# Optimization experiments

Measured on AMD Instinct MI355X. Metric: run time of the kernel, lower is better.

The kernel has to match this reference:

```python
import jax, jax.numpy as jnp
import numpy as np

B, N, C = 8, 1024, 768
H = 12
D = C // H  # head_dim = 64
SCALE = D ** -0.5


def setup_inputs() -> dict:
    key = jax.random.key(0)
    k1, k2, k3 = jax.random.split(key, 3)
    x = jax.random.normal(k1, (B, N, C), dtype=jnp.float32)
    # nn.Linear(dim, 3*dim, bias=False): weight [3C, C]
    w_qkv = jax.random.normal(k2, (3 * C, C), dtype=jnp.float32) * (C ** -0.5)
    # nn.Linear(dim, dim): weight [C, C], bias [C]
    w_proj = jax.random.normal(k3, (C, C), dtype=jnp.float32) * (C ** -0.5)
    b_proj = jnp.zeros((C,), dtype=jnp.float32)
    return {"x": x, "w_qkv": w_qkv, "w_proj": w_proj, "b_proj": b_proj}


def reference(x, w_qkv, w_proj, b_proj):
    b, n, c = x.shape
    # qkv projection: [B,N,3C] -> [3,B,H,N,D]
    qkv = jnp.einsum('bnc,fc->bnf', x, w_qkv)
    qkv = qkv.reshape(b, n, 3, H, D).transpose(2, 0, 3, 1, 4)
    q, k, v = qkv[0], qkv[1], qkv[2]
    # scaled dot-product attention (q scaled as in timm: q @ k^T * scale)
    attn = jnp.einsum('bhnd,bhmd->bhnm', q, k) * SCALE
    attn = jax.nn.softmax(attn, axis=-1)
    out = jnp.einsum('bhnm,bhmd->bhnd', attn, v)  # [B,H,N,D]
    out = out.transpose(0, 2, 1, 3).reshape(b, n, c)
    # output projection
    out = jnp.einsum('bnc,oc->bno', out, w_proj) + b_proj
    return out
```

## Files before the change

### kernel.cpp

```cpp
#include <hip/hip_runtime.h>
#include <hip/hip_bf16.h>
#include <stdint.h>


typedef unsigned short u16;
typedef __attribute__((ext_vector_type(8))) short    short8;
typedef __attribute__((ext_vector_type(4))) short    short4v;
typedef __attribute__((ext_vector_type(8))) __bf16   bf16x8;
typedef __attribute__((ext_vector_type(8))) unsigned short ushort8_t;
typedef __attribute__((ext_vector_type(4))) float    f32x4;

#define QSCALE 0.18033688011112042f

__device__ __forceinline__ u16 f2bf(float f) {
  union { float f; uint32_t u; } v; v.f = f;
  uint32_t u = v.u;
  u += 0x7fffu + ((u >> 16) & 1u);
  return (u16)(u >> 16);
}

__device__ __forceinline__ uint32_t pack_bf16(float hi, float lo) {
  uint32_t a = __builtin_bit_cast(uint32_t, hi) + 0x8000u;
  uint32_t b = __builtin_bit_cast(uint32_t, lo) + 0x8000u;
  return __builtin_amdgcn_perm(a, b, 0x07060302u);
}

__device__ __forceinline__ void gl_lds16(const void* g, void* l) {
  __builtin_amdgcn_global_load_lds(
      (const __attribute__((address_space(1))) void*)g,
      (__attribute__((address_space(3))) void*)l, 16, 0, 0);
}

__device__ __forceinline__ f32x4 mfma16(short8 a, short8 b, f32x4 c) {
  return __builtin_amdgcn_mfma_f32_16x16x32_bf16(
      __builtin_bit_cast(bf16x8, a), __builtin_bit_cast(bf16x8, b), c, 0, 0, 0);
}

__device__ __forceinline__ f32x4 mfma16k16(short4v a, short4v b, f32x4 c) {
#if __has_builtin(__builtin_amdgcn_mfma_f32_16x16x16bf16_1k)
  return __builtin_amdgcn_mfma_f32_16x16x16bf16_1k(a, b, c, 0, 0, 0);
#else
  f32x4 d = c;
  asm volatile("v_mfma_f32_16x16x16_bf16 %0, %1, %2, %0"
               : "+v"(d) : "v"(a), "v"(b));
  return d;
#endif
}

__global__ void cvt3_kernel(const float* __restrict__ x, const float* __restrict__ wq,
                            const float* __restrict__ wp, u16* __restrict__ dst) {
  const int i = blockIdx.x * blockDim.x + threadIdx.x;
  constexpr int NX = 6291456 / 4, NQ = 1769472 / 4, NP = 589824 / 4;
  float4 v;
  if (i < NX)                v = ((const float4*)x)[i];
  else if (i < NX + NQ)      v = ((const float4*)wq)[i - NX];
  else if (i < NX + NQ + NP) v = ((const float4*)wp)[i - NX - NQ];
  else return;
  ushort4 o;
  o.x = f2bf(v.x); o.y = f2bf(v.y); o.z = f2bf(v.z); o.w = f2bf(v.w);
  ((ushort4*)dst)[i] = o;
}

template <int NBX, int MODE>
__global__ __launch_bounds__(256)
void gemm_bt(const u16* __restrict__ A, const u16* __restrict__ Bw,
             u16* __restrict__ Qb, u16* __restrict__ Kb, u16* __restrict__ Vtb,
             float* __restrict__ outF, const float* __restrict__ bias) {
  constexpr int K = 768;
  __shared__ union {
    struct { alignas(16) u16 A[2][128 * 32]; alignas(16) u16 B[2][128 * 32]; } st;
    alignas(16) u16 vx[4][64 * 72];
  } sm;
  const int t = threadIdx.x;
  const int lane = t & 63;
  const int w = t >> 6;
  const int col = lane & 15;
  const int quad = lane >> 4;
  const int lin = blockIdx.x;
  const int xcd = lin & 7, j = lin >> 3;
  const int mi = xcd * 8 + (j & 7);
  const int ni = j >> 3;
  const int m0 = mi * 128;
  const int n0 = ni * 128;
  const int wm = (w >> 1) * 64;
  const int wn = (w & 1) * 64;

  f32x4 acc[4][4];
#pragma unroll
  for (int i = 0; i < 4; i++)
#pragma unroll
    for (int jj = 0; jj < 4; jj++) acc[i][jj] = (f32x4){0.f, 0.f, 0.f, 0.f};

  auto stage = [&](int buf, int k0) {
#pragma unroll
    for (int i = 0; i < 2; i++) {
      const int c = t + i * 256;
      const int row = c >> 2, kc = c & 3;
      gl_lds16(A + (m0 + row) * K + k0 + kc * 8, &sm.st.A[buf][c * 8]);
      gl_lds16(Bw + (n0 + row) * K + k0 + kc * 8, &sm.st.B[buf][c * 8]);
    }
  };

  stage(0, 0);
  for (int it = 0; it < K / 32; it++) {
    const int buf = it & 1;
    __syncthreads();
    if (it < K / 32 - 1) stage(buf ^ 1, (it + 1) * 32);
    short8 af[4], bf[4];
#pragma unroll
    for (int mb = 0; mb < 4; mb++)
      af[mb] = *(const short8*)&sm.st.A[buf][(wm + mb * 16 + col) * 32 + quad * 8];
#pragma unroll
    for (int nb = 0; nb < 4; nb++)
      bf[nb] = *(const short8*)&sm.st.B[buf][(wn + nb * 16 + col) * 32 + quad * 8];
#pragma unroll
    for (int mb = 0; mb < 4; mb++)
#pragma unroll
      for (int nb = 0; nb < 4; nb++)
        acc[mb][nb] = mfma16(af[mb], bf[nb], acc[mb][nb]);
  }

  if (MODE == 0) {
    const int tsel = n0 / 768;
    if (tsel == 2) {
      __syncthreads();
      u16* vx = sm.vx[w];
      const int b = (m0 + wm) >> 10;
      const int h = (n0 + wn - 1536) >> 6;
      const int nbase = ((m0 + wm) & 1023);
#pragma unroll
      for (int mb = 0; mb < 4; mb++)
#pragma unroll
        for (int nb = 0; nb < 4; nb++) {
          const int dloc = nb * 16 + col;
          const int tok = mb * 16 + quad * 4;
          uint2 pk;
          pk.x = pack_bf16(acc[mb][nb][1], acc[mb][nb][0]);
          pk.y = pack_bf16(acc[mb][nb][3], acc[mb][nb][2]);
          *(uint2*)&vx[dloc * 72 + tok] = pk;
        }
      __builtin_amdgcn_s_waitcnt(0);
#pragma unroll
      for (int i = 0; i < 8; i++) {
        const int dloc = i * 8 + (lane >> 3);
        const int tok = (lane & 7) * 8;
        ushort8_t v = *(const ushort8_t*)&vx[dloc * 72 + tok];
        *(ushort8_t*)&Vtb[((b * 12 + h) * 64 + dloc) * 1024 + nbase + tok] = v;
      }
    } else {
      u16* dst = (tsel == 0) ? Qb : Kb;
      const float scale = (tsel == 0) ? QSCALE : 1.0f;
#pragma unroll
      for (int mb = 0; mb < 4; mb++)
#pragma unroll
        for (int nb = 0; nb < 4; nb++)
#pragma unroll
          for (int r = 0; r < 4; r++) {
            const int row = m0 + wm + mb * 16 + quad * 4 + r;
            const int cc = n0 + wn + nb * 16 + col;
            const int b = row >> 10, n = row & 1023;
            const int hd = cc - tsel * 768;
            const int h = hd >> 6, d = hd & 63;
            dst[((b * 12 + h) * 1024 + n) * 64 + d] = f2bf(acc[mb][nb][r] * scale);
          }
    }
  } else {
#pragma unroll
    for (int mb = 0; mb < 4; mb++)
#pragma unroll
      for (int nb = 0; nb < 4; nb++)
#pragma unroll
        for (int r = 0; r < 4; r++) {
          const int row = m0 + wm + mb * 16 + quad * 4 + r;
          const int cc = n0 + wn + nb * 16 + col;
          outF[(size_t)row * 768 + cc] = acc[mb][nb][r] + bias[cc];
        }
  }
}

__global__ __launch_bounds__(256, 3)
void attn_kernel(const u16* __restrict__ Qb, const u16* __restrict__ Kb,
                 const u16* __restrict__ Vtb, u16* __restrict__ attnb) {
  __shared__ alignas(16) u16 Ks[2][64 * 64];
  __shared__ alignas(16) u16 Vs[2][64 * 64];
  const int t = threadIdx.x;
  const int lane = t & 63;
  const int w = t >> 6;
  const int col = lane & 15;
  const int quad = lane >> 4;
  const int lin = blockIdx.x;
  const int xcd = lin & 7, idx = lin >> 3;
  const int bh = xcd * 12 + idx % 12;
  const int qt = idx / 12;

  const u16* Qh = Qb + bh * 65536;
  const u16* Kh = Kb + bh * 65536;
  const u16* Vh = Vtb + bh * 65536;

  const int qrow0 = qt * 128 + w * 32;
  short8 qf[2][2];
#pragma unroll
  for (int g = 0; g < 2; g++)
#pragma unroll
    for (int s = 0; s < 2; s++)
      qf[g][s] = *(const short8*)&Qh[(qrow0 + g * 16 + col) * 64 + s * 32 + quad * 8];

  f32x4 oaccT[2][4];
#pragma unroll
  for (int g = 0; g < 2; g++)
#pragma unroll
    for (int nb = 0; nb < 4; nb++) oaccT[g][nb] = (f32x4){0.f, 0.f, 0.f, 0.f};
  float lacc[2] = {0.f, 0.f};

  auto stage = [&](int buf, int kt) {
#pragma unroll
    for (int i = 0; i < 2; i++) {
      const int c = t + i * 256;
      const int row = c >> 3, jj = c & 7;
      const int js = jj ^ (row & 7);
      gl_lds16(Kh + (kt * 64 + row) * 64 + js * 8, &Ks[buf][c * 8]);
      gl_lds16(Vh + row * 1024 + kt * 64 + js * 8, &Vs[buf][c * 8]);
    }
  };

  stage(0, 0);
  for (int kt = 0; kt < 16; kt++) {
    const int buf = kt & 1;
    __syncthreads();
    if (kt < 15) stage(buf ^ 1, kt + 1);

    f32x4 sv[2][4];
#pragma unroll
    for (int g = 0; g < 2; g++)
#pragma unroll
      for (int kb = 0; kb < 4; kb++) sv[g][kb] = (f32x4){0.f, 0.f, 0.f, 0.f};
#pragma unroll
    for (int kb = 0; kb < 4; kb++) {
      const int key = kb * 16 + col;
#pragma unroll
      for (int s = 0; s < 2; s++) {
        const short8 kf = *(const short8*)&Ks[buf][key * 64 + ((s * 4 + quad) ^ (key & 7)) * 8];
        sv[0][kb] = mfma16(kf, qf[0][s], sv[0][kb]);
        sv[1][kb] = mfma16(kf, qf[1][s], sv[1][kb]);
      }
    }

    short4v pfrag[2][4];
#pragma unroll
    for (int g = 0; g < 2; g++) {
      float ps = 0.f;
#pragma unroll
      for (int kb = 0; kb < 4; kb++) {
        const float p0 = exp2f(sv[g][kb][0]);
        const float p1 = exp2f(sv[g][kb][1]);
        const float p2 = exp2f(sv[g][kb][2]);
        const float p3 = exp2f(sv[g][kb][3]);
        ps += (p0 + p1) + (p2 + p3);
        uint2 pk = {pack_bf16(p1, p0), pack_bf16(p3, p2)};
        pfrag[g][kb] = __builtin_bit_cast(short4v, pk);
      }
      lacc[g] += ps;
    }

#pragma unroll
    for (int nb = 0; nb < 4; nb++) {
      const int d = nb * 16 + col;
#pragma unroll
      for (int kb = 0; kb < 4; kb++) {
        const int chunk = kb * 2 + (quad >> 1);
        const short4v vf = *(const short4v*)
            &Vs[buf][d * 64 + ((chunk ^ (d & 7)) * 8) + (quad & 1) * 4];
        oaccT[0][nb] = mfma16k16(vf, pfrag[0][kb], oaccT[0][nb]);
        oaccT[1][nb] = mfma16k16(vf, pfrag[1][kb], oaccT[1][nb]);
      }
    }
  }

  const int b = bh / 12, h = bh % 12;
#pragma unroll
  for (int g = 0; g < 2; g++) {
    float l = lacc[g];
    l += __shfl_xor(l, 16);
    l += __shfl_xor(l, 32);
    const float inv = 1.0f / l;
    const int n = qrow0 + g * 16 + col;
#pragma unroll
    for (int nb = 0; nb < 4; nb++) {
      const int cc = h * 64 + nb * 16 + quad * 4;
      uint2 pk;
      pk.x = pack_bf16(oaccT[g][nb][1] * inv, oaccT[g][nb][0] * inv);
      pk.y = pack_bf16(oaccT[g][nb][3] * inv, oaccT[g][nb][2] * inv);
      *(uint2*)&attnb[(b * 1024 + n) * 768 + cc] = pk;
    }
  }
}

extern "C" void kernel_launch(void* const* d_in, const int* in_sizes, int n_in,
                              void* d_out, int out_size, void* d_ws, size_t ws_size,
                              hipStream_t stream) {
  const float* x      = (const float*)d_in[0];
  const float* w_qkv  = (const float*)d_in[1];
  const float* w_proj = (const float*)d_in[2];
  const float* b_proj = (const float*)d_in[3];
  float* out = (float*)d_out;
  char* ws = (char*)d_ws;

  u16* xb    = (u16*)(ws + 0);
  u16* wqb   = (u16*)(ws + 12582912);
  u16* wpb   = (u16*)(ws + 16121856);
  u16* Qb    = (u16*)(ws + 17301504);
  u16* Kb    = (u16*)(ws + 29884416);
  u16* Vtb   = (u16*)(ws + 42467328);
  u16* attnb = (u16*)(ws + 0);

  cvt3_kernel<<<8448, 256, 0, stream>>>(x, w_qkv, w_proj, xb);
  gemm_bt<18, 0><<<1152, 256, 0, stream>>>(xb, wqb, Qb, Kb, Vtb, nullptr, nullptr);
  attn_kernel<<<768, 256, 0, stream>>>(Qb, Kb, Vtb, attnb);
  gemm_bt<6, 1><<<384, 256, 0, stream>>>(attnb, wpb, nullptr, nullptr, nullptr, out, b_proj);
}
```

Baseline: 126.7 us.

## Load K/V fragments directly from global into registers, drop LDS staging

The attention kernel no longer stages K and V tiles through double-buffered shared memory with block-wide barriers. Each wave now loads its MFMA operand fragments straight from global memory into registers and prefetches the next tile after each matmul phase. This removes the LDS traffic and __syncthreads, but the four waves of a block each fetch the same K/V data separately, which relies on L1/L2 cache and raises register pressure under the occupancy-3 launch bound. The V loads are strided by row, 16-byte and 8-byte, so coalescing may suffer.

After: 206.1 us. +62.6%, slower.

```diff
diff --git a/kernel.cpp b/kernel.cpp
--- a/kernel.cpp
+++ b/kernel.cpp
@@ -181,8 +181,6 @@
 __global__ __launch_bounds__(256, 3)
 void attn_kernel(const u16* __restrict__ Qb, const u16* __restrict__ Kb,
                  const u16* __restrict__ Vtb, u16* __restrict__ attnb) {
-  __shared__ alignas(16) u16 Ks[2][64 * 64];
-  __shared__ alignas(16) u16 Vs[2][64 * 64];
   const int t = threadIdx.x;
   const int lane = t & 63;
   const int w = t >> 6;
@@ -212,38 +210,42 @@
     for (int nb = 0; nb < 4; nb++) oaccT[g][nb] = (f32x4){0.f, 0.f, 0.f, 0.f};
   float lacc[2] = {0.f, 0.f};
 
-  auto stage = [&](int buf, int kt) {
-#pragma unroll
-    for (int i = 0; i < 2; i++) {
-      const int c = t + i * 256;
-      const int row = c >> 3, jj = c & 7;
-      const int js = jj ^ (row & 7);
-      gl_lds16(Kh + (kt * 64 + row) * 64 + js * 8, &Ks[buf][c * 8]);
-      gl_lds16(Vh + row * 1024 + kt * 64 + js * 8, &Vs[buf][c * 8]);
-    }
+  short8 kf[4][2];
+  short4v vf[4][4];
+  const u16* Kbase = Kh + col * 64 + quad * 8;
+  const u16* Vbase = Vh + col * 1024 + quad * 4;
+
+  auto loadK = [&](int kt) {
+#pragma unroll
+    for (int kb = 0; kb < 4; kb++)
+#pragma unroll
+      for (int s = 0; s < 2; s++)
+        kf[kb][s] = *(const short8*)&Kbase[kt * 4096 + kb * 1024 + s * 32];
   };
-
-  stage(0, 0);
+  auto loadV = [&](int kt) {
+#pragma unroll
+    for (int nb = 0; nb < 4; nb++)
+#pragma unroll
+      for (int kb = 0; kb < 4; kb++)
+        vf[nb][kb] = *(const short4v*)&Vbase[nb * 16384 + kt * 64 + kb * 16];
+  };
+
+  loadK(0);
+  loadV(0);
   for (int kt = 0; kt < 16; kt++) {
-    const int buf = kt & 1;
-    __syncthreads();
-    if (kt < 15) stage(buf ^ 1, kt + 1);
-
     f32x4 sv[2][4];
 #pragma unroll
     for (int g = 0; g < 2; g++)
 #pragma unroll
       for (int kb = 0; kb < 4; kb++) sv[g][kb] = (f32x4){0.f, 0.f, 0.f, 0.f};
 #pragma unroll
-    for (int kb = 0; kb < 4; kb++) {
-      const int key = kb * 16 + col;
+    for (int kb = 0; kb < 4; kb++)
 #pragma unroll
       for (int s = 0; s < 2; s++) {
-        const short8 kf = *(const short8*)&Ks[buf][key * 64 + ((s * 4 + quad) ^ (key & 7)) * 8];
-        sv[0][kb] = mfma16(kf, qf[0][s], sv[0][kb]);
-        sv[1][kb] = mfma16(kf, qf[1][s], sv[1][kb]);
+        sv[0][kb] = mfma16(kf[kb][s], qf[0][s], sv[0][kb]);
+        sv[1][kb] = mfma16(kf[kb][s], qf[1][s], sv[1][kb]);
       }
-    }
+    if (kt < 15) loadK(kt + 1);
 
     short4v pfrag[2][4];
 #pragma unroll
@@ -263,17 +265,13 @@
     }
 
 #pragma unroll
-    for (int nb = 0; nb < 4; nb++) {
-      const int d = nb * 16 + col;
+    for (int nb = 0; nb < 4; nb++)
 #pragma unroll
       for (int kb = 0; kb < 4; kb++) {
-        const int chunk = kb * 2 + (quad >> 1);
-        const short4v vf = *(const short4v*)
-            &Vs[buf][d * 64 + ((chunk ^ (d & 7)) * 8) + (quad & 1) * 4];
-        oaccT[0][nb] = mfma16k16(vf, pfrag[0][kb], oaccT[0][nb]);
-        oaccT[1][nb] = mfma16k16(vf, pfrag[1][kb], oaccT[1][nb]);
+        oaccT[0][nb] = mfma16k16(vf[nb][kb], pfrag[0][kb], oaccT[0][nb]);
+        oaccT[1][nb] = mfma16k16(vf[nb][kb], pfrag[1][kb], oaccT[1][nb]);
       }
-    }
+    if (kt < 15) loadV(kt + 1);
   }
 
   const int b = bh / 12, h = bh % 12;
```
